# Kernel optimization log

Hardware: AMD Instinct MI355X
Metric: run time of the kernel (lower is better)

The kernel has to match this reference:

```python
import jax, jax.numpy as jnp
import numpy as np

N_HEADS, BUCKET, N_HASHES, DIM = 8, 25, 4, 128
PKM_TOPK = 16
NEG = -1e9
SELF_VAL = -5e4

def layer_norm(x, g, b, eps=1e-5):
    m = jnp.mean(x, -1, keepdims=True)
    v = jnp.mean(jnp.square(x - m), -1, keepdims=True)
    return (x - m) * jax.lax.rsqrt(v + eps) * g + b

def pos_encoding(S, d):
    pos = jnp.arange(S, dtype=jnp.float32)[:, None]
    div = jnp.exp(jnp.arange(0, d, 2, dtype=jnp.float32) * (-9.21034037198 / d))
    pe = jnp.zeros((S, d), jnp.float32)
    pe = pe.at[:, 0::2].set(jnp.sin(pos * div))
    pe = pe.at[:, 1::2].set(jnp.cos(pos * div))
    return pe

def look_back(t):
    # concat each chunk with the previous chunk along the within-chunk axis
    return jnp.concatenate([t, jnp.roll(t, 1, axis=1)], axis=2)

def lsh_attend(qk, v, keep, rot):
    # qk, v: [BH, S, D]; keep: [BH, S] bool; rot: [D, R, n_buckets//2]
    BH, S, D = qk.shape
    R = rot.shape[1]
    nb = 2 * rot.shape[2]
    kn = qk * jax.lax.rsqrt(jnp.sum(jnp.square(qk), -1, keepdims=True) + 1e-9)  # shared-QK keys are unit length
    rotated = jnp.einsum('bsd,drn->brsn', qk, rot)
    buckets = jnp.argmax(jnp.concatenate([rotated, -rotated], -1), axis=-1)  # [BH, R, S]
    buckets = buckets + (jnp.arange(R) * nb)[None, :, None]  # offset per hash round
    buckets = buckets.reshape(BH, R * S)
    pos = jnp.arange(R * S) % S
    perm = jnp.argsort(buckets * S + pos[None, :], axis=-1)  # stable sort by (bucket, position)
    undo = jnp.argsort(perm, axis=-1)
    st = perm % S  # original token position of each sorted slot
    gather = lambda t: jnp.take_along_axis(t, st[:, :, None], axis=1)
    c = BUCKET
    nc = (R * S) // c
    sq = gather(qk).reshape(BH, nc, c, D)
    sk = gather(kn).reshape(BH, nc, c, D)
    sv = gather(v).reshape(BH, nc, c, D)
    sm = jnp.take_along_axis(keep, st, axis=1).reshape(BH, nc, c)
    t_q = st.reshape(BH, nc, c)
    bk, bv = look_back(sk), look_back(sv)
    t_kv, m_kv = look_back(t_q), look_back(sm)
    dots = jnp.einsum('bncd,bnkd->bnck', sq, bk) * (D ** -0.5)  # [BH, nc, c, 2c]
    pair = sm[..., :, None] & m_kv[..., None, :]
    dots = jnp.where(pair, dots, NEG)                                   # padding mask
    dots = jnp.where(t_q[..., :, None] < t_kv[..., None, :], NEG, dots)  # causal
    dots = jnp.where(t_q[..., :, None] == t_kv[..., None, :], SELF_VAL, dots)  # discourage self-attn
    lse = jax.nn.logsumexp(dots, axis=-1, keepdims=True)
    attn = jnp.exp(dots - lse)
    bo = jnp.einsum('bnck,bnkd->bncd', attn, bv)
    so = bo.reshape(BH, R * S, D)
    slse = lse.reshape(BH, R * S)
    o = jnp.take_along_axis(so, undo[:, :, None], axis=1).reshape(BH, R, S, D)
    lu = jnp.take_along_axis(slse, undo, axis=1).reshape(BH, R, S)
    w = jax.nn.softmax(lu, axis=1)[..., None]  # combine hash rounds by their logsumexp
    return jnp.sum(o * w, axis=1)

def lsh_self_attention(x, keep, Wqk, Wv, Wo, bo, rot):
    B, S, dim = x.shape
    H = N_HEADS
    Dh = dim // H
    split = lambda t: t.reshape(B, S, H, Dh).transpose(0, 2, 1, 3).reshape(B * H, S, Dh)
    qk, v = split(x @ Wqk), split(x @ Wv)
    keep_bh = jnp.repeat(keep, H, axis=0)
    o = lsh_attend(qk, v, keep_bh, rot)
    o = o.reshape(B, H, S, Dh).transpose(0, 2, 1, 3).reshape(B, S, dim)
    return o @ Wo + bo

def pkm(x, Wq, keys, values):
    # keys: [H, nk, 2, dh]; values: [nk*nk, dim] (product-key memory)
    B, S, dim = x.shape
    H, nk, _, dh = keys.shape
    q = (x @ Wq).reshape(B, S, H, 2, dh)
    dots = jnp.einsum('bshpd,hnpd->bshpn', q, keys)
    sx, ix = jax.lax.top_k(dots[..., 0, :], PKM_TOPK)
    sy, iy = jax.lax.top_k(dots[..., 1, :], PKM_TOPK)
    alls = (sx[..., :, None] + sy[..., None, :]).reshape(B, S, H, PKM_TOPK * PKM_TOPK)
    alli = (ix[..., :, None] * nk + iy[..., None, :]).reshape(B, S, H, PKM_TOPK * PKM_TOPK)
    fs, p = jax.lax.top_k(alls, PKM_TOPK)
    fi = jnp.take_along_axis(alli, p, axis=-1)
    attn = jax.nn.softmax(fs, -1)
    return jnp.einsum('bshk,bshkd->bsd', attn, values[fi])

def model_forward(fl, xi):
    (emb_mcc, emb_amt, emb_hour, emb_wday, rot, ln1_g, ln1_b, ln2_g, ln2_b,
     Wqk, Wv, Wo, bo, ff_w1, ff_b1, ff_w2, ff_b2, pkm_wq, pkm_keys, pkm_values,
     norm_g, norm_b, hw1, hb1, hw2_mcc, hb2_mcc, hw2_amt, hb2_amt,
     hw2_hour, hb2_hour, hw2_wday, hb2_wday) = fl
    x_mcc, x_amt, x_hour, x_wday = xi
    B, S = x_mcc.shape
    emb = jnp.concatenate([emb_mcc[x_mcc], emb_amt[x_amt], emb_hour[x_hour], emb_wday[x_wday]], axis=-1)
    emb = emb + pos_encoding(S, DIM)[None]
    keep = x_mcc != 0
    # reversible reformer: x1 = x1 + attn(ln(x2)); x2 = x2 + ff_or_pkm(ln(x1)); out = mean of halves
    x1 = x2 = emb
    ffi = pki = 0
    for l in range(8):
        h = layer_norm(x2, ln1_g[l], ln1_b[l])
        x1 = x1 + lsh_self_attention(h, keep, Wqk[l], Wv[l], Wo[l], bo[l], rot)
        h2 = layer_norm(x1, ln2_g[l], ln2_b[l])
        if l in (3, 6):  # pkm_layers = (4, 7), 1-indexed
            x2 = x2 + pkm(h2, pkm_wq[pki], pkm_keys[pki], pkm_values[pki])
            pki += 1
        else:
            x2 = x2 + (jax.nn.gelu(h2 @ ff_w1[ffi] + ff_b1[ffi], approximate=False) @ ff_w2[ffi] + ff_b2[ffi])
            ffi += 1
    y = layer_norm((x1 + x2) * 0.5, norm_g, norm_b)
    outs = []
    for i, (w2, b2) in enumerate([(hw2_mcc, hb2_mcc), (hw2_amt, hb2_amt), (hw2_hour, hb2_hour), (hw2_wday, hb2_wday)]):
        h = jax.nn.gelu(y @ hw1[i] + hb1[i], approximate=False)
        outs.append(h @ w2 + b2)
    return tuple(outs)

def setup_inputs() -> dict:
    key = jax.random.key(0)
    ks = iter(jax.random.split(key, 64))
    B, S = 16, 1000
    nrm = lambda *s: jax.random.normal(next(ks), s, jnp.float32) * 0.02
    inp = dict(
        x_mcc=jax.random.randint(next(ks), (B, S), 0, 350),
        x_amt=jax.random.randint(next(ks), (B, S), 0, 100),
        x_hour=jax.random.randint(next(ks), (B, S), 0, 25),
        x_wday=jax.random.randint(next(ks), (B, S), 0, 8),
        emb_mcc=nrm(350, 64), emb_amt=nrm(100, 32), emb_hour=nrm(25, 16), emb_wday=nrm(8, 16),
        rot=jax.random.normal(next(ks), (16, N_HASHES, 20), jnp.float32),  # [dim_head, rounds, n_buckets//2]
        ln1_g=jnp.ones((8, 128)), ln1_b=jnp.zeros((8, 128)),
        ln2_g=jnp.ones((8, 128)), ln2_b=jnp.zeros((8, 128)),
        Wqk=nrm(8, 128, 128), Wv=nrm(8, 128, 128), Wo=nrm(8, 128, 128), bo=jnp.zeros((8, 128)),
        ff_w1=nrm(6, 128, 512), ff_b1=jnp.zeros((6, 512)), ff_w2=nrm(6, 512, 128), ff_b2=jnp.zeros((6, 128)),
        pkm_wq=nrm(2, 128, 512), pkm_keys=nrm(2, 4, 128, 2, 64), pkm_values=nrm(2, 16384, 128),
        norm_g=jnp.ones((128,)), norm_b=jnp.zeros((128,)),
        hw1=nrm(4, 128, 128), hb1=jnp.zeros((4, 128)),
        hw2_mcc=nrm(128, 350), hb2_mcc=jnp.zeros((350,)),
        hw2_amt=nrm(128, 100), hb2_amt=jnp.zeros((100,)),
        hw2_hour=nrm(128, 25), hb2_hour=jnp.zeros((25,)),
        hw2_wday=nrm(128, 8), hb2_wday=jnp.zeros((8,)),
    )
    return inp

def reference(x_mcc, x_amt, x_hour, x_wday, emb_mcc, emb_amt, emb_hour, emb_wday, rot,
              ln1_g, ln1_b, ln2_g, ln2_b, Wqk, Wv, Wo, bo,
              ff_w1, ff_b1, ff_w2, ff_b2, pkm_wq, pkm_keys, pkm_values,
              norm_g, norm_b, hw1, hb1, hw2_mcc, hb2_mcc, hw2_amt, hb2_amt,
              hw2_hour, hb2_hour, hw2_wday, hb2_wday):
    fl = (emb_mcc, emb_amt, emb_hour, emb_wday, rot, ln1_g, ln1_b, ln2_g, ln2_b,
          Wqk, Wv, Wo, bo, ff_w1, ff_b1, ff_w2, ff_b2, pkm_wq, pkm_keys, pkm_values,
          norm_g, norm_b, hw1, hb1, hw2_mcc, hb2_mcc, hw2_amt, hb2_amt,
          hw2_hour, hb2_hour, hw2_wday, hb2_wday)
    return model_forward(fl, (x_mcc, x_amt, x_hour, x_wday))
```

## Files before the change

### kernel.cpp

```cpp
#include <hip/hip_runtime.h>
#include <math.h>

#define MM_GELU 1
#define MM_RES 2
#define MM_SPLIT 4

typedef __attribute__((ext_vector_type(8))) short bfrag;
typedef __attribute__((ext_vector_type(4))) float f32x4;

__device__ inline unsigned short f2bf_rne(float f) {
  unsigned u = __float_as_uint(f);
  unsigned r = u + 0x7FFFu + ((u >> 16) & 1u);
  return (unsigned short)(r >> 16);
}
__device__ inline float bf2f(unsigned short h) {
  return __uint_as_float(((unsigned)h) << 16);
}

__global__ __launch_bounds__(128) void embed_kernel(
    const int* __restrict__ xm, const int* __restrict__ xa,
    const int* __restrict__ xh, const int* __restrict__ xw,
    const float* __restrict__ em, const float* __restrict__ ea,
    const float* __restrict__ eh, const float* __restrict__ ew,
    float* __restrict__ x1, float* __restrict__ x2) {
  int row = blockIdx.x;
  int d = threadIdx.x;
  int s = row % 1000;
  float v;
  if (d < 64)       v = em[xm[row]*64 + d];
  else if (d < 96)  v = ea[xa[row]*32 + (d-64)];
  else if (d < 112) v = eh[xh[row]*16 + (d-96)];
  else              v = ew[xw[row]*16 + (d-112)];
  int i = d >> 1;
  float dv = expf((float)(2*i) * (-9.21034037198f/128.f));
  float ang = (float)s * dv;
  v += (d & 1) ? cosf(ang) : sinf(ang);
  x1[row*128 + d] = v;
  x2[row*128 + d] = v;
}

__global__ __launch_bounds__(256) void ln_kernel(
    const float* __restrict__ x, const float* __restrict__ xb,
    const float* __restrict__ g, const float* __restrict__ b,
    float* __restrict__ out) {
  int row = blockIdx.x * 4 + (threadIdx.x >> 6);
  int t = threadIdx.x & 63;
  float v0 = x[row*128 + t], v1 = x[row*128 + 64 + t];
  if (xb) { v0 = 0.5f*(v0 + xb[row*128 + t]); v1 = 0.5f*(v1 + xb[row*128 + 64 + t]); }
  float sum = v0 + v1;
  #pragma unroll
  for (int o = 32; o > 0; o >>= 1) sum += __shfl_xor(sum, o);
  float mean = sum * (1.f/128.f);
  float d0 = v0 - mean, d1 = v1 - mean;
  float vs = d0*d0 + d1*d1;
  #pragma unroll
  for (int o = 32; o > 0; o >>= 1) vs += __shfl_xor(vs, o);
  float rstd = rsqrtf(vs*(1.f/128.f) + 1e-5f);
  out[row*128 + t]      = d0*rstd*g[t]    + b[t];
  out[row*128 + 64 + t] = d1*rstd*g[t+64] + b[t+64];
}

__global__ __launch_bounds__(256) void mfma_matmul_kernel(
    const float* __restrict__ A, const float* __restrict__ W,
    const float* __restrict__ bias, float* __restrict__ C,
    int M, int N, int K, int flags) {
  __shared__ __align__(16) unsigned short Ah[64*40], Al[64*40], Bh[64*40], Bl[64*40];
  int tid = threadIdx.x;
  int bm = blockIdx.x * 64, bn = blockIdx.y * 64;
  int w = tid >> 6, lane = tid & 63;
  int l15 = lane & 15, kg = lane >> 4;
  f32x4 acc[4];
  #pragma unroll
  for (int t = 0; t < 4; ++t) { acc[t][0]=0.f; acc[t][1]=0.f; acc[t][2]=0.f; acc[t][3]=0.f; }
  int arr = tid >> 2, akc = (tid & 3) * 8;
  int bcol = tid >> 2, bk0 = (tid & 3) * 8;

  for (int k0 = 0; k0 < K; k0 += 32) {
    {
      const float* ap = A + (size_t)(bm + arr) * K + k0 + akc;
      float4 fa = *(const float4*)(ap);
      float4 fb = *(const float4*)(ap + 4);
      float av8[8] = {fa.x, fa.y, fa.z, fa.w, fb.x, fb.y, fb.z, fb.w};
      bfrag vh, vl;
      #pragma unroll
      for (int j = 0; j < 8; ++j) {
        unsigned short h = f2bf_rne(av8[j]);
        vh[j] = (short)h;
        vl[j] = (short)f2bf_rne(av8[j] - bf2f(h));
      }
      *(bfrag*)&Ah[arr*40 + akc] = vh;
      *(bfrag*)&Al[arr*40 + akc] = vl;
    }
    {
      int c = bn + bcol;
      float bv8[8];
      #pragma unroll
      for (int j = 0; j < 8; ++j) {
        int kk = k0 + bk0 + j;
        bv8[j] = (c < N) ? W[(size_t)kk * N + c] : 0.f;
      }
      #pragma unroll
      for (int j = 0; j < 8; j += 2) {
        unsigned short h0 = f2bf_rne(bv8[j]),   h1 = f2bf_rne(bv8[j+1]);
        unsigned short l0 = f2bf_rne(bv8[j]   - bf2f(h0));
        unsigned short l1 = f2bf_rne(bv8[j+1] - bf2f(h1));
        *(unsigned*)&Bh[bcol*40 + bk0 + j] = ((unsigned)h1 << 16) | h0;
        *(unsigned*)&Bl[bcol*40 + bk0 + j] = ((unsigned)l1 << 16) | l0;
      }
    }
    __syncthreads();
    int am = w*16 + l15;
    bfrag a_h = *(const bfrag*)&Ah[am*40 + kg*8];
    bfrag a_l = *(const bfrag*)&Al[am*40 + kg*8];
    #pragma unroll
    for (int t = 0; t < 4; ++t) {
      int nn = t*16 + l15;
      bfrag b_h = *(const bfrag*)&Bh[nn*40 + kg*8];
      bfrag b_l = *(const bfrag*)&Bl[nn*40 + kg*8];
      acc[t] = __builtin_amdgcn_mfma_f32_16x16x32_bf16(a_h, b_h, acc[t], 0, 0, 0);
      acc[t] = __builtin_amdgcn_mfma_f32_16x16x32_bf16(a_h, b_l, acc[t], 0, 0, 0);
      acc[t] = __builtin_amdgcn_mfma_f32_16x16x32_bf16(a_l, b_h, acc[t], 0, 0, 0);
    }
    __syncthreads();
  }
  #pragma unroll
  for (int t = 0; t < 4; ++t) {
    int col = bn + t*16 + l15;
    if (col < N) {
      #pragma unroll
      for (int r = 0; r < 4; ++r) {
        int row = bm + w*16 + kg*4 + r;
        float val = acc[t][r];
        if (bias) val += bias[col];
        if (flags & MM_GELU) val = 0.5f*val*(1.f + erff(val*0.70710678118f));
        size_t oi;
        if (flags & MM_SPLIT) {
          int bb = row / 1000, ss = row % 1000;
          int hd = col >> 4, dd = col & 15;
          oi = (((size_t)(bb*8 + hd))*1000 + ss)*16 + dd;
        } else {
          oi = (size_t)row*N + col;
        }
        if (flags & MM_RES) C[oi] += val; else C[oi] = val;
      }
    }
  }
}

__global__ __launch_bounds__(256) void bucket_kernel(
    const float* __restrict__ qk, const float* __restrict__ rot,
    int* __restrict__ buckets) {
  int idx = blockIdx.x*256 + threadIdx.x;
  if (idx >= 128000) return;
  int bh = idx / 1000, s = idx % 1000;
  float q[16];
  #pragma unroll
  for (int d = 0; d < 16; ++d) q[d] = qk[(bh*1000+s)*16 + d];
  #pragma unroll 1
  for (int r = 0; r < 4; ++r) {
    float rv[20];
    #pragma unroll
    for (int n = 0; n < 20; ++n) {
      float acc = 0.f;
      #pragma unroll
      for (int d = 0; d < 16; ++d) acc += q[d]*rot[(d*4 + r)*20 + n];
      rv[n] = acc;
    }
    float best = -INFINITY; int bi = 0;
    #pragma unroll
    for (int n = 0; n < 40; ++n) {
      float val = (n < 20) ? rv[n] : -rv[n-20];
      if (val > best) { best = val; bi = n; }
    }
    buckets[(bh*4 + r)*1000 + s] = bi;
  }
}

__global__ __launch_bounds__(64) void sort_kernel(
    const int* __restrict__ buckets, int* __restrict__ st, int* __restrict__ undo) {
  int bh = blockIdx.x >> 2;
  int r = blockIdx.x & 3;
  const int* bkt = buckets + (bh*4 + r)*1000;
  __shared__ int off[40];
  int lane = threadIdx.x;
  if (lane < 40) off[lane] = 0;
  __syncthreads();
  unsigned long long below = (lane == 63) ? 0x7FFFFFFFFFFFFFFFull : ((1ull << lane) - 1ull);
  for (int c = 0; c < 16; ++c) {
    int s = c*64 + lane;
    bool valid = (s < 1000);
    int b = valid ? bkt[s] : 0;
    unsigned long long mask = __ballot(valid);
    #pragma unroll
    for (int bit = 0; bit < 6; ++bit) {
      unsigned long long vote = __ballot((b >> bit) & 1);
      mask &= ((b >> bit) & 1) ? vote : ~vote;
    }
    if (valid) {
      int rank = (int)__popcll(mask & below);
      if (rank == 0) off[b] += (int)__popcll(mask);
    }
    __syncthreads();
  }
  if (lane == 0) {
    int acc = 0;
    for (int bb = 0; bb < 40; ++bb) { int cn = off[bb]; off[bb] = acc; acc += cn; }
  }
  __syncthreads();
  int base = bh*4000 + r*1000;
  for (int c = 0; c < 16; ++c) {
    int s = c*64 + lane;
    bool valid = (s < 1000);
    int b = valid ? bkt[s] : 0;
    unsigned long long mask = __ballot(valid);
    #pragma unroll
    for (int bit = 0; bit < 6; ++bit) {
      unsigned long long vote = __ballot((b >> bit) & 1);
      mask &= ((b >> bit) & 1) ? vote : ~vote;
    }
    if (valid) {
      int myoff = off[b];
      int rank = (int)__popcll(mask & below);
      int slot = myoff + rank;
      st[base + slot] = s;
      undo[base + s] = r*1000 + slot;
      if (rank == 0) off[b] = myoff + (int)__popcll(mask);
    }
    __syncthreads();
  }
}

__global__ __launch_bounds__(64) void attn_chunk_kernel(
    const float* __restrict__ qk, const float* __restrict__ v,
    const int* __restrict__ st, const int* __restrict__ xm,
    float* __restrict__ so, float* __restrict__ slse) {
  int blk = blockIdx.x;
  int bh = blk / 160;
  int n = blk % 160;
  int b = bh >> 3;
  int lane = threadIdx.x;
  __shared__ __align__(16) float RAW[50][20];
  __shared__ __align__(16) float BV[50][20];
  __shared__ float RSQ[50];
  __shared__ int TKV[50], MKV[50];
  int pn = (n + 159) % 160;
  if (lane < 50) {
    int slot = (lane < 25) ? (n*25 + lane) : (pn*25 + (lane - 25));
    int t = st[bh*4000 + slot];
    TKV[lane] = t;
    MKV[lane] = (xm[b*1000 + t] != 0) ? 1 : 0;
  }
  __syncthreads();
  for (int e = lane; e < 200; e += 64) {
    int rr = e >> 2, j = (e & 3) * 4;
    int t = TKV[rr];
    const float* qr = qk + ((size_t)bh*1000 + t)*16 + j;
    const float* vr = v  + ((size_t)bh*1000 + t)*16 + j;
    *(float4*)&RAW[rr][j] = *(const float4*)qr;
    *(float4*)&BV[rr][j]  = *(const float4*)vr;
  }
  __syncthreads();
  if (lane < 50) {
    float ss = 1e-9f;
    #pragma unroll
    for (int d = 0; d < 16; ++d) ss += RAW[lane][d]*RAW[lane][d];
    RSQ[lane] = rsqrtf(ss);
  }
  __syncthreads();
  if (lane < 50) {
    int q = lane % 25, h = lane / 25;
    int partner = (h == 0) ? lane + 25 : lane - 25;
    float sq[16];
    #pragma unroll
    for (int j = 0; j < 4; ++j) {
      float4 f = *(const float4*)&RAW[q][j*4];
      sq[j*4+0]=f.x; sq[j*4+1]=f.y; sq[j*4+2]=f.z; sq[j*4+3]=f.w;
    }
    int tq = TKV[q], mq = MKV[q];
    float p[25];
    #pragma unroll
    for (int i = 0; i < 25; ++i) {
      int k = h*25 + i;
      float acc = 0.f;
      #pragma unroll
      for (int j = 0; j < 4; ++j) {
        float4 f = *(const float4*)&RAW[k][j*4];
        acc += sq[j*4+0]*f.x + sq[j*4+1]*f.y + sq[j*4+2]*f.z + sq[j*4+3]*f.w;
      }
      acc *= 0.25f * RSQ[k];
      int tk = TKV[k], mk = MKV[k];
      if (!(mq && mk)) acc = -1e9f;
      if (tq < tk) acc = -1e9f;
      if (tq == tk) acc = -5e4f;
      p[i] = acc;
    }
    float m = -INFINITY;
    #pragma unroll
    for (int i = 0; i < 25; ++i) m = fmaxf(m, p[i]);
    m = fmaxf(m, __shfl(m, partner));
    float S = 0.f;
    #pragma unroll
    for (int i = 0; i < 25; ++i) { p[i] = expf(p[i] - m); S += p[i]; }
    S += __shfl(S, partner);
    float lse = m + logf(S);
    float rS = 1.f / S;
    float o[16];
    #pragma unroll
    for (int d = 0; d < 16; ++d) o[d] = 0.f;
    #pragma unroll
    for (int i = 0; i < 25; ++i) {
      int k = h*25 + i;
      float wt = p[i];
      #pragma unroll
      for (int j = 0; j < 4; ++j) {
        float4 f = *(const float4*)&BV[k][j*4];
        o[j*4+0] += wt*f.x; o[j*4+1] += wt*f.y; o[j*4+2] += wt*f.z; o[j*4+3] += wt*f.w;
      }
    }
    #pragma unroll
    for (int d = 0; d < 16; ++d) o[d] += __shfl(o[d], partner);
    if (h == 0) {
      int slot = n*25 + q;
      float* op = so + ((size_t)bh*4000 + slot)*16;
      #pragma unroll
      for (int j = 0; j < 4; ++j) {
        float4 f;
        f.x = o[j*4+0]*rS; f.y = o[j*4+1]*rS; f.z = o[j*4+2]*rS; f.w = o[j*4+3]*rS;
        *(float4*)(op + j*4) = f;
      }
      slse[bh*4000 + slot] = lse;
    }
  }
}

__global__ __launch_bounds__(256) void combine_kernel(
    const float* __restrict__ so, const float* __restrict__ slse,
    const int* __restrict__ undo, float* __restrict__ ao) {
  int idx = blockIdx.x*256 + threadIdx.x;
  if (idx >= 2048000) return;
  int d = idx & 15;
  int s = (idx >> 4) % 1000;
  int bh = idx / 16000;
  int b = bh >> 3, hd = bh & 7;
  int s0 = undo[bh*4000 + s];
  int s1 = undo[bh*4000 + 1000 + s];
  int s2 = undo[bh*4000 + 2000 + s];
  int s3 = undo[bh*4000 + 3000 + s];
  float l0 = slse[bh*4000 + s0], l1 = slse[bh*4000 + s1];
  float l2 = slse[bh*4000 + s2], l3 = slse[bh*4000 + s3];
  float m = fmaxf(fmaxf(l0,l1), fmaxf(l2,l3));
  float w0 = expf(l0-m), w1 = expf(l1-m), w2 = expf(l2-m), w3 = expf(l3-m);
  float rs = 1.f/(w0+w1+w2+w3);
  const float* base = so + (size_t)bh*4000*16;
  float o = w0*base[s0*16+d] + w1*base[s1*16+d] + w2*base[s2*16+d] + w3*base[s3*16+d];
  ao[((size_t)b*1000 + s)*128 + hd*16 + d] = o * rs;
}

__global__ __launch_bounds__(256) void pkm_m_kernel(
    const float* __restrict__ Wq, const float* __restrict__ keys,
    float* __restrict__ M) {
  int hp = blockIdx.x;
  int h = hp >> 1, p = hp & 1;
  int tid = threadIdx.x;
  __shared__ float Ks[128][65];
  for (int e = tid; e < 8192; e += 256) {
    int n = e >> 6, d = e & 63;
    Ks[n][d] = keys[((size_t)(h*128 + n)*2 + p)*64 + d];
  }
  __syncthreads();
  int k = tid >> 1;
  int nbase = (tid & 1) * 64;
  float wk[64];
  const float* wq = Wq + (size_t)k*512 + h*128 + p*64;
  #pragma unroll
  for (int d = 0; d < 64; ++d) wk[d] = wq[d];
  for (int n = 0; n < 64; ++n) {
    int nn = nbase + n;
    float acc = 0.f;
    #pragma unroll
    for (int d = 0; d < 64; ++d) acc += wk[d]*Ks[nn][d];
    M[(size_t)k*1024 + hp*128 + nn] = acc;
  }
}

__device__ inline unsigned long long pk_key(float v, int idx) {
  unsigned u = __float_as_uint(v);
  u = (u & 0x80000000u) ? ~u : (u | 0x80000000u);
  unsigned kv = ~u;
  return ((unsigned long long)kv << 32) | (unsigned)idx;
}
__device__ inline float pk_val(unsigned long long key) {
  unsigned m = ~(unsigned)(key >> 32);
  return (m & 0x80000000u) ? __uint_as_float(m & 0x7FFFFFFFu) : __uint_as_float(~m);
}

__global__ __launch_bounds__(512) void pkm_select_kernel(
    const float* __restrict__ dots, const float* __restrict__ values,
    float* __restrict__ x2out) {
  int row = blockIdx.x;
  int tid = threadIdx.x;
  int w = tid >> 6;
  int lane = tid & 63;
  int h = w >> 1, p = w & 1;
  __shared__ float SVAL[4][2][16];
  __shared__ int SIDX[4][2][16];
  __shared__ float OUT[4][128];
  const float* dr = dots + (size_t)row*1024 + h*256 + p*128;
  {
    unsigned long long k0 = pk_key(dr[lane], lane);
    unsigned long long k1 = pk_key(dr[64 + lane], 64 + lane);
    #pragma unroll 1
    for (int k = 2; k <= 128; k <<= 1) {
      #pragma unroll 1
      for (int j = k >> 1; j >= 1; j >>= 1) {
        if (j == 64) {
          unsigned long long lo = (k0 < k1) ? k0 : k1;
          unsigned long long hi = (k0 < k1) ? k1 : k0;
          k0 = lo; k1 = hi;
        } else {
          unsigned long long p0 = __shfl_xor(k0, j);
          unsigned long long p1 = __shfl_xor(k1, j);
          bool low = ((lane & j) == 0);
          bool up0 = ((lane & k) == 0);
          bool up1 = (((lane + 64) & k) == 0);
          bool t0 = (low == up0) ? (p0 < k0) : (p0 > k0);
          bool t1 = (low == up1) ? (p1 < k1) : (p1 > k1);
          if (t0) k0 = p0;
          if (t1) k1 = p1;
        }
      }
    }
    if (lane < 16) {
      SVAL[h][p][lane] = pk_val(k0);
      SIDX[h][p][lane] = (int)(unsigned)(k0 & 0xFFFFFFFFull);
    }
  }
  __syncthreads();
  if (p == 0) {
    int kx, ky;
    if      (lane < 16) { kx = 0; ky = lane; }
    else if (lane < 24) { kx = 1; ky = lane - 16; }
    else if (lane < 29) { kx = 2; ky = lane - 24; }
    else if (lane < 33) { kx = 3; ky = lane - 29; }
    else if (lane < 36) { kx = 4; ky = lane - 33; }
    else if (lane < 38) { kx = 5; ky = lane - 36; }
    else if (lane < 40) { kx = 6; ky = lane - 38; }
    else if (lane < 42) { kx = 7; ky = lane - 40; }
    else                { kx = 8 + (lane - 42); ky = 0; }
    unsigned long long key;
    if (lane < 50) {
      float cv = SVAL[h][0][kx] + SVAL[h][1][ky];
      key = pk_key(cv, kx*16 + ky);
    } else {
      key = ~0ull;
    }
    #pragma unroll 1
    for (int k = 2; k <= 64; k <<= 1) {
      #pragma unroll 1
      for (int j = k >> 1; j >= 1; j >>= 1) {
        unsigned long long pk = __shfl_xor(key, j);
        bool low = ((lane & j) == 0);
        bool up = ((lane & k) == 0);
        bool take = (low == up) ? (pk < key) : (pk > key);
        if (take) key = pk;
      }
    }
    float myv = pk_val(key);
    int pos = (int)(key & 0xFFull);
    int myfi = SIDX[h][0][pos >> 4] * 128 + SIDX[h][1][pos & 15];
    float fs0 = __shfl(myv, 0);
    float osum0 = 0.f, osum1 = 0.f, wsum = 0.f;
    #pragma unroll
    for (int k = 0; k < 16; ++k) {
      float fv = __shfl(myv, k);
      int fik = __shfl(myfi, k);
      float wgk = expf(fv - fs0);
      wsum += wgk;
      const float* vr = values + (size_t)fik * 128;
      osum0 += wgk * vr[lane];
      osum1 += wgk * vr[lane + 64];
    }
    float rs = 1.f / wsum;
    OUT[h][lane] = osum0 * rs;
    OUT[h][lane + 64] = osum1 * rs;
  }
  __syncthreads();
  if (tid < 128) {
    float r = OUT[0][tid] + OUT[1][tid] + OUT[2][tid] + OUT[3][tid];
    x2out[(size_t)row*128 + tid] += r;
  }
}

extern "C" void kernel_launch(void* const* d_in, const int* in_sizes, int n_in,
                              void* d_out, int out_size, void* d_ws, size_t ws_size,
                              hipStream_t stream) {
  (void)in_sizes; (void)n_in; (void)out_size; (void)ws_size;
  const int* x_mcc  = (const int*)d_in[0];
  const int* x_amt  = (const int*)d_in[1];
  const int* x_hour = (const int*)d_in[2];
  const int* x_wday = (const int*)d_in[3];
  const float* emb_mcc  = (const float*)d_in[4];
  const float* emb_amt  = (const float*)d_in[5];
  const float* emb_hour = (const float*)d_in[6];
  const float* emb_wday = (const float*)d_in[7];
  const float* rot   = (const float*)d_in[8];
  const float* ln1_g = (const float*)d_in[9];
  const float* ln1_b = (const float*)d_in[10];
  const float* ln2_g = (const float*)d_in[11];
  const float* ln2_b = (const float*)d_in[12];
  const float* Wqk = (const float*)d_in[13];
  const float* Wv  = (const float*)d_in[14];
  const float* Wo  = (const float*)d_in[15];
  const float* bo  = (const float*)d_in[16];
  const float* ff_w1 = (const float*)d_in[17];
  const float* ff_b1 = (const float*)d_in[18];
  const float* ff_w2 = (const float*)d_in[19];
  const float* ff_b2 = (const float*)d_in[20];
  const float* pkm_wq   = (const float*)d_in[21];
  const float* pkm_keys = (const float*)d_in[22];
  const float* pkm_vals = (const float*)d_in[23];
  const float* norm_g = (const float*)d_in[24];
  const float* norm_b = (const float*)d_in[25];
  const float* hw1 = (const float*)d_in[26];
  const float* hb1 = (const float*)d_in[27];

  float* ws = (float*)d_ws;
  float* x1v  = ws;
  float* x2v  = ws + 2048000;
  float* hbuf = ws + 4096000;
  float* scrA = ws + 6144000;
  float* qk     = scrA;
  float* vv     = scrA + 2048000;
  float* so     = scrA + 4096000;
  float* slse   = scrA + 12288000;
  int*   buckets= (int*)(scrA + 12800000);
  int*   stp    = (int*)(scrA + 13312000);
  int*   undo   = (int*)(scrA + 13824000);
  float* attn_o = scrA + 14336000;
  float* big    = scrA;
  float* dotsb  = scrA;
  float* Mbuf   = ws + 22528000;

  embed_kernel<<<16000, 128, 0, stream>>>(x_mcc, x_amt, x_hour, x_wday,
      emb_mcc, emb_amt, emb_hour, emb_wday, x1v, x2v);

  int ffi = 0, pki = 0;
  for (int l = 0; l < 8; ++l) {
    ln_kernel<<<4000, 256, 0, stream>>>(x2v, nullptr, ln1_g + l*128, ln1_b + l*128, hbuf);
    { dim3 g(250, 2); mfma_matmul_kernel<<<g, 256, 0, stream>>>(hbuf, Wqk + (size_t)l*16384, nullptr, qk, 16000, 128, 128, MM_SPLIT); }
    { dim3 g(250, 2); mfma_matmul_kernel<<<g, 256, 0, stream>>>(hbuf, Wv  + (size_t)l*16384, nullptr, vv, 16000, 128, 128, MM_SPLIT); }
    bucket_kernel<<<500, 256, 0, stream>>>(qk, rot, buckets);
    sort_kernel<<<512, 64, 0, stream>>>(buckets, stp, undo);
    attn_chunk_kernel<<<20480, 64, 0, stream>>>(qk, vv, stp, x_mcc, so, slse);
    combine_kernel<<<8000, 256, 0, stream>>>(so, slse, undo, attn_o);
    { dim3 g(250, 2); mfma_matmul_kernel<<<g, 256, 0, stream>>>(attn_o, Wo + (size_t)l*16384, bo + l*128, x1v, 16000, 128, 128, MM_RES); }
    ln_kernel<<<4000, 256, 0, stream>>>(x1v, nullptr, ln2_g + l*128, ln2_b + l*128, hbuf);
    if (l == 3 || l == 6) {
      pkm_m_kernel<<<8, 256, 0, stream>>>(pkm_wq + (size_t)pki*65536, pkm_keys + (size_t)pki*65536, Mbuf);
      { dim3 g(250, 16); mfma_matmul_kernel<<<g, 256, 0, stream>>>(hbuf, Mbuf, nullptr, dotsb, 16000, 1024, 128, 0); }
      pkm_select_kernel<<<16000, 512, 0, stream>>>(dotsb, pkm_vals + (size_t)pki*2097152, x2v);
      ++pki;
    } else {
      { dim3 g(250, 8); mfma_matmul_kernel<<<g, 256, 0, stream>>>(hbuf, ff_w1 + (size_t)ffi*65536, ff_b1 + ffi*512, big, 16000, 512, 128, MM_GELU); }
      { dim3 g(250, 2); mfma_matmul_kernel<<<g, 256, 0, stream>>>(big, ff_w2 + (size_t)ffi*65536, ff_b2 + ffi*128, x2v, 16000, 128, 512, MM_RES); }
      ++ffi;
    }
  }
  ln_kernel<<<4000, 256, 0, stream>>>(x1v, x2v, norm_g, norm_b, hbuf);

  float* out = (float*)d_out;
  float* hid = scrA;
  const float* w2s[4] = {(const float*)d_in[28], (const float*)d_in[30], (const float*)d_in[32], (const float*)d_in[34]};
  const float* b2s[4] = {(const float*)d_in[29], (const float*)d_in[31], (const float*)d_in[33], (const float*)d_in[35]};
  const int ns[4] = {350, 100, 25, 8};
  size_t ooff = 0;
  for (int i = 0; i < 4; ++i) {
    { dim3 g(250, 2); mfma_matmul_kernel<<<g, 256, 0, stream>>>(hbuf, hw1 + (size_t)i*16384, hb1 + i*128, hid, 16000, 128, 128, MM_GELU); }
    { dim3 g(250, (unsigned)((ns[i]+63)/64)); mfma_matmul_kernel<<<g, 256, 0, stream>>>(hid, w2s[i], b2s[i], out + ooff, 16000, ns[i], 128, 0); }
    ooff += (size_t)16000 * ns[i];
  }
}
```

Before: 2.557 ms.

## Pre-split weights and activations into bf16 hi/lo, transpose weights, simplify PKM select

```diff
diff --git a/kernel.cpp b/kernel.cpp
--- a/kernel.cpp
+++ b/kernel.cpp
@@ -4,6 +4,7 @@
 #define MM_GELU 1
 #define MM_RES 2
 #define MM_SPLIT 4
+#define MM_SPLITONLY 8
 
 typedef __attribute__((ext_vector_type(8))) short bfrag;
 typedef __attribute__((ext_vector_type(4))) float f32x4;
@@ -42,7 +43,7 @@
 __global__ __launch_bounds__(256) void ln_kernel(
     const float* __restrict__ x, const float* __restrict__ xb,
     const float* __restrict__ g, const float* __restrict__ b,
-    float* __restrict__ out) {
+    unsigned short* __restrict__ oh, unsigned short* __restrict__ ol) {
   int row = blockIdx.x * 4 + (threadIdx.x >> 6);
   int t = threadIdx.x & 63;
   float v0 = x[row*128 + t], v1 = x[row*128 + 64 + t];
@@ -56,15 +57,52 @@
   #pragma unroll
   for (int o = 32; o > 0; o >>= 1) vs += __shfl_xor(vs, o);
   float rstd = rsqrtf(vs*(1.f/128.f) + 1e-5f);
-  out[row*128 + t]      = d0*rstd*g[t]    + b[t];
-  out[row*128 + 64 + t] = d1*rstd*g[t+64] + b[t+64];
-}
-
-__global__ __launch_bounds__(256) void mfma_matmul_kernel(
-    const float* __restrict__ A, const float* __restrict__ W,
+  float y0 = d0*rstd*g[t]    + b[t];
+  float y1 = d1*rstd*g[t+64] + b[t+64];
+  unsigned short h0 = f2bf_rne(y0), h1 = f2bf_rne(y1);
+  oh[row*128 + t]      = h0;
+  ol[row*128 + t]      = f2bf_rne(y0 - bf2f(h0));
+  oh[row*128 + 64 + t] = h1;
+  ol[row*128 + 64 + t] = f2bf_rne(y1 - bf2f(h1));
+}
+
+__global__ __launch_bounds__(256) void splitT_kernel(
+    const float* __restrict__ src, unsigned short* __restrict__ hiT,
+    unsigned short* __restrict__ loT, int K, int N,
+    long srcStride, long dstStride) {
+  src += (size_t)blockIdx.z * srcStride;
+  hiT += (size_t)blockIdx.z * dstStride;
+  loT += (size_t)blockIdx.z * dstStride;
+  int n0 = blockIdx.x * 64, k0 = blockIdx.y * 64;
+  __shared__ unsigned short sH[64][68], sL[64][68];
+  int tid = threadIdx.x;
+  int c = tid & 63, r4 = tid >> 6;
+  #pragma unroll
+  for (int rr = 0; rr < 16; ++rr) {
+    int r = r4 + rr*4;
+    float val = (n0 + c < N) ? src[(size_t)(k0 + r)*N + n0 + c] : 0.f;
+    unsigned short h = f2bf_rne(val);
+    sH[r][c] = h;
+    sL[r][c] = f2bf_rne(val - bf2f(h));
+  }
+  __syncthreads();
+  #pragma unroll
+  for (int rr = 0; rr < 16; ++rr) {
+    int n = r4 + rr*4;
+    if (n0 + n < N) {
+      hiT[(size_t)(n0 + n)*K + k0 + c] = sH[c][n];
+      loT[(size_t)(n0 + n)*K + k0 + c] = sL[c][n];
+    }
+  }
+}
+
+__global__ __launch_bounds__(256) void mm_bf16_kernel(
+    const unsigned short* __restrict__ Ah, const unsigned short* __restrict__ Al,
+    const unsigned short* __restrict__ BhT, const unsigned short* __restrict__ BlT,
     const float* __restrict__ bias, float* __restrict__ C,
+    unsigned short* __restrict__ Ch, unsigned short* __restrict__ Cl,
     int M, int N, int K, int flags) {
-  __shared__ __align__(16) unsigned short Ah[64*40], Al[64*40], Bh[64*40], Bl[64*40];
+  __shared__ __align__(16) unsigned short sAh[64][72], sAl[64][72], sBh[64][72], sBl[64][72];
   int tid = threadIdx.x;
   int bm = blockIdx.x * 64, bn = blockIdx.y * 64;
   int w = tid >> 6, lane = tid & 63;
@@ -72,54 +110,41 @@
   f32x4 acc[4];
   #pragma unroll
   for (int t = 0; t < 4; ++t) { acc[t][0]=0.f; acc[t][1]=0.f; acc[t][2]=0.f; acc[t][3]=0.f; }
-  int arr = tid >> 2, akc = (tid & 3) * 8;
-  int bcol = tid >> 2, bk0 = (tid & 3) * 8;
-
-  for (int k0 = 0; k0 < K; k0 += 32) {
-    {
-      const float* ap = A + (size_t)(bm + arr) * K + k0 + akc;
-      float4 fa = *(const float4*)(ap);
-      float4 fb = *(const float4*)(ap + 4);
-      float av8[8] = {fa.x, fa.y, fa.z, fa.w, fb.x, fb.y, fb.z, fb.w};
-      bfrag vh, vl;
+
+  for (int k0 = 0; k0 < K; k0 += 64) {
+    #pragma unroll
+    for (int uu = 0; uu < 2; ++uu) {
+      int u = tid + uu*256;
+      int rr = u >> 3, cc = u & 7;
+      size_t ga = (size_t)(bm + rr)*K + k0 + cc*8;
+      *(bfrag*)&sAh[rr][cc*8] = *(const bfrag*)(Ah + ga);
+      *(bfrag*)&sAl[rr][cc*8] = *(const bfrag*)(Al + ga);
+      int n = bn + rr;
+      if (n < N) {
+        size_t gb = (size_t)n*K + k0 + cc*8;
+        *(bfrag*)&sBh[rr][cc*8] = *(const bfrag*)(BhT + gb);
+        *(bfrag*)&sBl[rr][cc*8] = *(const bfrag*)(BlT + gb);
+      } else {
+        bfrag z = {0,0,0,0,0,0,0,0};
+        *(bfrag*)&sBh[rr][cc*8] = z;
+        *(bfrag*)&sBl[rr][cc*8] = z;
+      }
+    }
+    __syncthreads();
+    #pragma unroll
+    for (int ks = 0; ks < 2; ++ks) {
+      int am = w*16 + l15;
+      bfrag a_h = *(const bfrag*)&sAh[am][ks*32 + kg*8];
+      bfrag a_l = *(const bfrag*)&sAl[am][ks*32 + kg*8];
       #pragma unroll
-      for (int j = 0; j < 8; ++j) {
-        unsigned short h = f2bf_rne(av8[j]);
-        vh[j] = (short)h;
-        vl[j] = (short)f2bf_rne(av8[j] - bf2f(h));
+      for (int t = 0; t < 4; ++t) {
+        int nn = t*16 + l15;
+        bfrag b_h = *(const bfrag*)&sBh[nn][ks*32 + kg*8];
+        bfrag b_l = *(const bfrag*)&sBl[nn][ks*32 + kg*8];
+        acc[t] = __builtin_amdgcn_mfma_f32_16x16x32_bf16(a_h, b_h, acc[t], 0, 0, 0);
+        acc[t] = __builtin_amdgcn_mfma_f32_16x16x32_bf16(a_h, b_l, acc[t], 0, 0, 0);
+        acc[t] = __builtin_amdgcn_mfma_f32_16x16x32_bf16(a_l, b_h, acc[t], 0, 0, 0);
       }
-      *(bfrag*)&Ah[arr*40 + akc] = vh;
-      *(bfrag*)&Al[arr*40 + akc] = vl;
-    }
-    {
-      int c = bn + bcol;
-      float bv8[8];
-      #pragma unroll
-      for (int j = 0; j < 8; ++j) {
-        int kk = k0 + bk0 + j;
-        bv8[j] = (c < N) ? W[(size_t)kk * N + c] : 0.f;
-      }
-      #pragma unroll
-      for (int j = 0; j < 8; j += 2) {
-        unsigned short h0 = f2bf_rne(bv8[j]),   h1 = f2bf_rne(bv8[j+1]);
-        unsigned short l0 = f2bf_rne(bv8[j]   - bf2f(h0));
-        unsigned short l1 = f2bf_rne(bv8[j+1] - bf2f(h1));
-        *(unsigned*)&Bh[bcol*40 + bk0 + j] = ((unsigned)h1 << 16) | h0;
-        *(unsigned*)&Bl[bcol*40 + bk0 + j] = ((unsigned)l1 << 16) | l0;
-      }
-    }
-    __syncthreads();
-    int am = w*16 + l15;
-    bfrag a_h = *(const bfrag*)&Ah[am*40 + kg*8];
-    bfrag a_l = *(const bfrag*)&Al[am*40 + kg*8];
-    #pragma unroll
-    for (int t = 0; t < 4; ++t) {
-      int nn = t*16 + l15;
-      bfrag b_h = *(const bfrag*)&Bh[nn*40 + kg*8];
-      bfrag b_l = *(const bfrag*)&Bl[nn*40 + kg*8];
-      acc[t] = __builtin_amdgcn_mfma_f32_16x16x32_bf16(a_h, b_h, acc[t], 0, 0, 0);
-      acc[t] = __builtin_amdgcn_mfma_f32_16x16x32_bf16(a_h, b_l, acc[t], 0, 0, 0);
-      acc[t] = __builtin_amdgcn_mfma_f32_16x16x32_bf16(a_l, b_h, acc[t], 0, 0, 0);
     }
     __syncthreads();
   }
@@ -141,7 +166,12 @@
         } else {
           oi = (size_t)row*N + col;
         }
-        if (flags & MM_RES) C[oi] += val; else C[oi] = val;
+        if (flags & MM_SPLITONLY) {
+          unsigned short h = f2bf_rne(val);
+          Ch[oi] = h;
+          Cl[oi] = f2bf_rne(val - bf2f(h));
+        } else if (flags & MM_RES) C[oi] += val;
+        else C[oi] = val;
       }
     }
   }
@@ -335,7 +365,8 @@
 
 __global__ __launch_bounds__(256) void combine_kernel(
     const float* __restrict__ so, const float* __restrict__ slse,
-    const int* __restrict__ undo, float* __restrict__ ao) {
+    const int* __restrict__ undo, unsigned short* __restrict__ aoh,
+    unsigned short* __restrict__ aol) {
   int idx = blockIdx.x*256 + threadIdx.x;
   if (idx >= 2048000) return;
   int d = idx & 15;
@@ -352,8 +383,11 @@
   float w0 = expf(l0-m), w1 = expf(l1-m), w2 = expf(l2-m), w3 = expf(l3-m);
   float rs = 1.f/(w0+w1+w2+w3);
   const float* base = so + (size_t)bh*4000*16;
-  float o = w0*base[s0*16+d] + w1*base[s1*16+d] + w2*base[s2*16+d] + w3*base[s3*16+d];
-  ao[((size_t)b*1000 + s)*128 + hd*16 + d] = o * rs;
+  float o = (w0*base[s0*16+d] + w1*base[s1*16+d] + w2*base[s2*16+d] + w3*base[s3*16+d]) * rs;
+  size_t oi = ((size_t)b*1000 + s)*128 + hd*16 + d;
+  unsigned short h = f2bf_rne(o);
+  aoh[oi] = h;
+  aol[oi] = f2bf_rne(o - bf2f(h));
 }
 
 __global__ __launch_bounds__(256) void pkm_m_kernel(
@@ -394,96 +428,92 @@
   return (m & 0x80000000u) ? __uint_as_float(m & 0x7FFFFFFFu) : __uint_as_float(~m);
 }
 
-__global__ __launch_bounds__(512) void pkm_select_kernel(
+__global__ __launch_bounds__(256) void pkm_select_kernel(
     const float* __restrict__ dots, const float* __restrict__ values,
     float* __restrict__ x2out) {
   int row = blockIdx.x;
   int tid = threadIdx.x;
-  int w = tid >> 6;
+  int h = tid >> 6;
   int lane = tid & 63;
-  int h = w >> 1, p = w & 1;
-  __shared__ float SVAL[4][2][16];
-  __shared__ int SIDX[4][2][16];
   __shared__ float OUT[4][128];
-  const float* dr = dots + (size_t)row*1024 + h*256 + p*128;
-  {
-    unsigned long long k0 = pk_key(dr[lane], lane);
-    unsigned long long k1 = pk_key(dr[64 + lane], 64 + lane);
+  const float* dr = dots + (size_t)row*1024 + h*256;
+  unsigned long long x0 = pk_key(dr[lane], lane);
+  unsigned long long x1 = pk_key(dr[64 + lane], 64 + lane);
+  unsigned long long y0 = pk_key(dr[128 + lane], lane);
+  unsigned long long y1 = pk_key(dr[192 + lane], 64 + lane);
+  #pragma unroll 1
+  for (int k = 2; k <= 128; k <<= 1) {
     #pragma unroll 1
-    for (int k = 2; k <= 128; k <<= 1) {
-      #pragma unroll 1
-      for (int j = k >> 1; j >= 1; j >>= 1) {
-        if (j == 64) {
-          unsigned long long lo = (k0 < k1) ? k0 : k1;
-          unsigned long long hi = (k0 < k1) ? k1 : k0;
-          k0 = lo; k1 = hi;
-        } else {
-          unsigned long long p0 = __shfl_xor(k0, j);
-          unsigned long long p1 = __shfl_xor(k1, j);
-          bool low = ((lane & j) == 0);
-          bool up0 = ((lane & k) == 0);
-          bool up1 = (((lane + 64) & k) == 0);
-          bool t0 = (low == up0) ? (p0 < k0) : (p0 > k0);
-          bool t1 = (low == up1) ? (p1 < k1) : (p1 > k1);
-          if (t0) k0 = p0;
-          if (t1) k1 = p1;
-        }
+    for (int j = k >> 1; j >= 1; j >>= 1) {
+      if (j == 64) {
+        unsigned long long lo, hi;
+        lo = (x0 < x1) ? x0 : x1; hi = (x0 < x1) ? x1 : x0; x0 = lo; x1 = hi;
+        lo = (y0 < y1) ? y0 : y1; hi = (y0 < y1) ? y1 : y0; y0 = lo; y1 = hi;
+      } else {
+        unsigned long long px0 = __shfl_xor(x0, j);
+        unsigned long long px1 = __shfl_xor(x1, j);
+        unsigned long long py0 = __shfl_xor(y0, j);
+        unsigned long long py1 = __shfl_xor(y1, j);
+        bool low = ((lane & j) == 0);
+        bool up0 = ((lane & k) == 0);
+        bool up1 = (((lane + 64) & k) == 0);
+        bool d0 = (low == up0);
+        bool d1 = (low == up1);
+        if (d0 ? (px0 < x0) : (px0 > x0)) x0 = px0;
+        if (d1 ? (px1 < x1) : (px1 > x1)) x1 = px1;
+        if (d0 ? (py0 < y0) : (py0 > y0)) y0 = py0;
+        if (d1 ? (py1 < y1) : (py1 > y1)) y1 = py1;
       }
     }
-    if (lane < 16) {
-      SVAL[h][p][lane] = pk_val(k0);
-      SIDX[h][p][lane] = (int)(unsigned)(k0 & 0xFFFFFFFFull);
-    }
-  }
-  __syncthreads();
-  if (p == 0) {
-    int kx, ky;
-    if      (lane < 16) { kx = 0; ky = lane; }
-    else if (lane < 24) { kx = 1; ky = lane - 16; }
-    else if (lane < 29) { kx = 2; ky = lane - 24; }
-    else if (lane < 33) { kx = 3; ky = lane - 29; }
-    else if (lane < 36) { kx = 4; ky = lane - 33; }
-    else if (lane < 38) { kx = 5; ky = lane - 36; }
-    else if (lane < 40) { kx = 6; ky = lane - 38; }
-    else if (lane < 42) { kx = 7; ky = lane - 40; }
-    else                { kx = 8 + (lane - 42); ky = 0; }
-    unsigned long long key;
-    if (lane < 50) {
-      float cv = SVAL[h][0][kx] + SVAL[h][1][ky];
-      key = pk_key(cv, kx*16 + ky);
-    } else {
-      key = ~0ull;
-    }
+  }
+  float xv = pk_val(x0);
+  float yv = pk_val(y0);
+  int xi = (int)(unsigned)(x0 & 0xFFFFFFFFull);
+  int yi = (int)(unsigned)(y0 & 0xFFFFFFFFull);
+  int kx, ky;
+  if      (lane < 16) { kx = 0; ky = lane; }
+  else if (lane < 24) { kx = 1; ky = lane - 16; }
+  else if (lane < 29) { kx = 2; ky = lane - 24; }
+  else if (lane < 33) { kx = 3; ky = lane - 29; }
+  else if (lane < 36) { kx = 4; ky = lane - 33; }
+  else if (lane < 38) { kx = 5; ky = lane - 36; }
+  else if (lane < 40) { kx = 6; ky = lane - 38; }
+  else if (lane < 42) { kx = 7; ky = lane - 40; }
+  else                { kx = 8 + (lane - 42); ky = 0; }
+  float sxk = __shfl(xv, kx);
+  float syk = __shfl(yv, ky);
+  unsigned long long key = (lane < 50) ? pk_key(sxk + syk, kx*16 + ky) : ~0ull;
+  #pragma unroll 1
+  for (int k = 2; k <= 64; k <<= 1) {
     #pragma unroll 1
-    for (int k = 2; k <= 64; k <<= 1) {
-      #pragma unroll 1
-      for (int j = k >> 1; j >= 1; j >>= 1) {
-        unsigned long long pk = __shfl_xor(key, j);
-        bool low = ((lane & j) == 0);
-        bool up = ((lane & k) == 0);
-        bool take = (low == up) ? (pk < key) : (pk > key);
-        if (take) key = pk;
-      }
-    }
-    float myv = pk_val(key);
-    int pos = (int)(key & 0xFFull);
-    int myfi = SIDX[h][0][pos >> 4] * 128 + SIDX[h][1][pos & 15];
-    float fs0 = __shfl(myv, 0);
-    float osum0 = 0.f, osum1 = 0.f, wsum = 0.f;
-    #pragma unroll
-    for (int k = 0; k < 16; ++k) {
-      float fv = __shfl(myv, k);
-      int fik = __shfl(myfi, k);
-      float wgk = expf(fv - fs0);
-      wsum += wgk;
-      const float* vr = values + (size_t)fik * 128;
-      osum0 += wgk * vr[lane];
-      osum1 += wgk * vr[lane + 64];
-    }
-    float rs = 1.f / wsum;
-    OUT[h][lane] = osum0 * rs;
-    OUT[h][lane + 64] = osum1 * rs;
-  }
+    for (int j = k >> 1; j >= 1; j >>= 1) {
+      unsigned long long pk = __shfl_xor(key, j);
+      bool low = ((lane & j) == 0);
+      bool up = ((lane & k) == 0);
+      bool take = (low == up) ? (pk < key) : (pk > key);
+      if (take) key = pk;
+    }
+  }
+  float myv = pk_val(key);
+  int pos = (int)(key & 0xFFull);
+  int ix = __shfl(xi, pos >> 4);
+  int iy = __shfl(yi, pos & 15);
+  int myfi = ix*128 + iy;
+  float fs0 = __shfl(myv, 0);
+  float osum0 = 0.f, osum1 = 0.f, wsum = 0.f;
+  #pragma unroll
+  for (int k = 0; k < 16; ++k) {
+    float fv = __shfl(myv, k);
+    int fik = __shfl(myfi, k);
+    float wgk = expf(fv - fs0);
+    wsum += wgk;
+    const float* vr = values + (size_t)fik * 128;
+    osum0 += wgk * vr[lane];
+    osum1 += wgk * vr[lane + 64];
+  }
+  float rs = 1.f / wsum;
+  OUT[h][lane] = osum0 * rs;
+  OUT[h][lane + 64] = osum1 * rs;
   __syncthreads();
   if (tid < 128) {
     float r = OUT[0][tid] + OUT[1][tid] + OUT[2][tid] + OUT[3][tid];
@@ -537,46 +567,84 @@
   int*   stp    = (int*)(scrA + 13312000);
   int*   undo   = (int*)(scrA + 13824000);
   float* attn_o = scrA + 14336000;
-  float* big    = scrA;
   float* dotsb  = scrA;
   float* Mbuf   = ws + 22528000;
 
+  unsigned short* hbuf_h = (unsigned short*)hbuf;
+  unsigned short* hbuf_l = hbuf_h + 2048000;
+  unsigned short* ao_h = (unsigned short*)attn_o;
+  unsigned short* ao_l = ao_h + 2048000;
+  unsigned short* big_h = (unsigned short*)scrA;
+  unsigned short* big_l = big_h + 8192000;
+  unsigned short* hid_h = ao_h;
+  unsigned short* hid_l = ao_l;
+
+  unsigned short* wsp = (unsigned short*)(ws + 22700000);
+  unsigned short* WqkT_h = wsp;
+  unsigned short* WqkT_l = wsp + 131072;
+  unsigned short* WvT_h  = wsp + 262144;
+  unsigned short* WvT_l  = wsp + 393216;
+  unsigned short* WoT_h  = wsp + 524288;
+  unsigned short* WoT_l  = wsp + 655360;
+  unsigned short* f1T_h  = wsp + 786432;
+  unsigned short* f1T_l  = wsp + 1179648;
+  unsigned short* f2T_h  = wsp + 1572864;
+  unsigned short* f2T_l  = wsp + 1966080;
+  unsigned short* MT_h   = wsp + 2359296;
+  unsigned short* MT_l   = wsp + 2490368;
+  unsigned short* hw1T_h = wsp + 2621440;
+  unsigned short* hw1T_l = wsp + 2686976;
+  unsigned short* h2T_h  = wsp + 2752512;
+  unsigned short* h2T_l  = wsp + 2814336;
+
+  { dim3 g(2,2,8); splitT_kernel<<<g,256,0,stream>>>(Wqk, WqkT_h, WqkT_l, 128,128, 16384,16384); }
+  { dim3 g(2,2,8); splitT_kernel<<<g,256,0,stream>>>(Wv,  WvT_h,  WvT_l,  128,128, 16384,16384); }
+  { dim3 g(2,2,8); splitT_kernel<<<g,256,0,stream>>>(Wo,  WoT_h,  WoT_l,  128,128, 16384,16384); }
+  { dim3 g(8,2,6); splitT_kernel<<<g,256,0,stream>>>(ff_w1, f1T_h, f1T_l, 128,512, 65536,65536); }
+  { dim3 g(2,8,6); splitT_kernel<<<g,256,0,stream>>>(ff_w2, f2T_h, f2T_l, 512,128, 65536,65536); }
+  { dim3 g(2,2,4); splitT_kernel<<<g,256,0,stream>>>(hw1, hw1T_h, hw1T_l, 128,128, 16384,16384); }
+  const float* w2s[4] = {(const float*)d_in[28], (const float*)d_in[30], (const float*)d_in[32], (const float*)d_in[34]};
+  const float* b2s[4] = {(const float*)d_in[29], (const float*)d_in[31], (const float*)d_in[33], (const float*)d_in[35]};
+  const int ns[4] = {350, 100, 25, 8};
+  const long h2off[4] = {0, 44800, 57600, 60800};
+  for (int i = 0; i < 4; ++i) {
+    dim3 g((ns[i]+63)/64, 2, 1);
+    splitT_kernel<<<g,256,0,stream>>>(w2s[i], h2T_h + h2off[i], h2T_l + h2off[i], 128, ns[i], 0, 0);
+  }
+
   embed_kernel<<<16000, 128, 0, stream>>>(x_mcc, x_amt, x_hour, x_wday,
       emb_mcc, emb_amt, emb_hour, emb_wday, x1v, x2v);
 
   int ffi = 0, pki = 0;
   for (int l = 0; l < 8; ++l) {
-    ln_kernel<<<4000, 256, 0, stream>>>(x2v, nullptr, ln1_g + l*128, ln1_b + l*128, hbuf);
-    { dim3 g(250, 2); mfma_matmul_kernel<<<g, 256, 0, stream>>>(hbuf, Wqk + (size_t)l*16384, nullptr, qk, 16000, 128, 128, MM_SPLIT); }
-    { dim3 g(250, 2); mfma_matmul_kernel<<<g, 256, 0, stream>>>(hbuf, Wv  + (size_t)l*16384, nullptr, vv, 16000, 128, 128, MM_SPLIT); }
+    ln_kernel<<<4000, 256, 0, stream>>>(x2v, nullptr, ln1_g + l*128, ln1_b + l*128, hbuf_h, hbuf_l);
+    { dim3 g(250, 2); mm_bf16_kernel<<<g, 256, 0, stream>>>(hbuf_h, hbuf_l, WqkT_h + l*16384, WqkT_l + l*16384, nullptr, qk, nullptr, nullptr, 16000, 128, 128, MM_SPLIT); }
+    { dim3 g(250, 2); mm_bf16_kernel<<<g, 256, 0, stream>>>(hbuf_h, hbuf_l, WvT_h + l*16384, WvT_l + l*16384, nullptr, vv, nullptr, nullptr, 16000, 128, 128, MM_SPLIT); }
     bucket_kernel<<<500, 256, 0, stream>>>(qk, rot, buckets);
     sort_kernel<<<512, 64, 0, stream>>>(buckets, stp, undo);
     attn_chunk_kernel<<<20480, 64, 0, stream>>>(qk, vv, stp, x_mcc, so, slse);
-    combine_kernel<<<8000, 256, 0, stream>>>(so, slse, undo, attn_o);
-    { dim3 g(250, 2); mfma_matmul_kernel<<<g, 256, 0, stream>>>(attn_o, Wo + (size_t)l*16384, bo + l*128, x1v, 16000, 128, 128, MM_RES); }
-    ln_kernel<<<4000, 256, 0, stream>>>(x1v, nullptr, ln2_g + l*128, ln2_b + l*128, hbuf);
+    combine_kernel<<<8000, 256, 0, stream>>>(so, slse, undo, ao_h, ao_l);
+    { dim3 g(250, 2); mm_bf16_kernel<<<g, 256, 0, stream>>>(ao_h, ao_l, WoT_h + l*16384, WoT_l + l*16384, bo + l*128, x1v, nullptr, nullptr, 16000, 128, 128, MM_RES); }
+    ln_kernel<<<4000, 256, 0, stream>>>(x1v, nullptr, ln2_g + l*128, ln2_b + l*128, hbuf_h, hbuf_l);
     if (l == 3 || l == 6) {
       pkm_m_kernel<<<8, 256, 0, stream>>>(pkm_wq + (size_t)pki*65536, pkm_keys + (size_t)pki*65536, Mbuf);
-      { dim3 g(250, 16); mfma_matmul_kernel<<<g, 256, 0, stream>>>(hbuf, Mbuf, nullptr, dotsb, 16000, 1024, 128, 0); }
-      pkm_select_kernel<<<16000, 512, 0, stream>>>(dotsb, pkm_vals + (size_t)pki*2097152, x2v);
+      { dim3 g(16, 2, 1); splitT_kernel<<<g,256,0,stream>>>(Mbuf, MT_h, MT_l, 128, 1024, 0, 0); }
+      { dim3 g(250, 16); mm_bf16_kernel<<<g, 256, 0, stream>>>(hbuf_h, hbuf_l, MT_h, MT_l, nullptr, dotsb, nullptr, nullptr, 16000, 1024, 128, 0); }
+      pkm_select_kernel<<<16000, 256, 0, stream>>>(dotsb, pkm_vals + (size_t)pki*2097152, x2v);
       ++pki;
     } else {
-      { dim3 g(250, 8); mfma_matmul_kernel<<<g, 256, 0, stream>>>(hbuf, ff_w1 + (size_t)ffi*65536, ff_b1 + ffi*512, big, 16000, 512, 128, MM_GELU); }
-      { dim3 g(250, 2); mfma_matmul_kernel<<<g, 256, 0, stream>>>(big, ff_w2 + (size_t)ffi*65536, ff_b2 + ffi*128, x2v, 16000, 128, 512, MM_RES); }
+      { dim3 g(250, 8); mm_bf16_kernel<<<g, 256, 0, stream>>>(hbuf_h, hbuf_l, f1T_h + ffi*65536, f1T_l + ffi*65536, ff_b1 + ffi*512, nullptr, big_h, big_l, 16000, 512, 128, MM_GELU|MM_SPLITONLY); }
+      { dim3 g(250, 2); mm_bf16_kernel<<<g, 256, 0, stream>>>(big_h, big_l, f2T_h + ffi*65536, f2T_l + ffi*65536, ff_b2 + ffi*128, x2v, nullptr, nullptr, 16000, 128, 512, MM_RES); }
       ++ffi;
     }
   }
-  ln_kernel<<<4000, 256, 0, stream>>>(x1v, x2v, norm_g, norm_b, hbuf);
+  ln_kernel<<<4000, 256, 0, stream>>>(x1v, x2v, norm_g, norm_b, hbuf_h, hbuf_l);
 
   float* out = (float*)d_out;
-  float* hid = scrA;
-  const float* w2s[4] = {(const float*)d_in[28], (const float*)d_in[30], (const float*)d_in[32], (const float*)d_in[34]};
-  const float* b2s[4] = {(const float*)d_in[29], (const float*)d_in[31], (const float*)d_in[33], (const float*)d_in[35]};
-  const int ns[4] = {350, 100, 25, 8};
   size_t ooff = 0;
   for (int i = 0; i < 4; ++i) {
-    { dim3 g(250, 2); mfma_matmul_kernel<<<g, 256, 0, stream>>>(hbuf, hw1 + (size_t)i*16384, hb1 + i*128, hid, 16000, 128, 128, MM_GELU); }
-    { dim3 g(250, (unsigned)((ns[i]+63)/64)); mfma_matmul_kernel<<<g, 256, 0, stream>>>(hid, w2s[i], b2s[i], out + ooff, 16000, ns[i], 128, 0); }
+    { dim3 g(250, 2); mm_bf16_kernel<<<g, 256, 0, stream>>>(hbuf_h, hbuf_l, hw1T_h + i*16384, hw1T_l + i*16384, hb1 + i*128, nullptr, hid_h, hid_l, 16000, 128, 128, MM_GELU|MM_SPLITONLY); }
+    { dim3 g(250, (unsigned)((ns[i]+63)/64)); mm_bf16_kernel<<<g, 256, 0, stream>>>(hid_h, hid_l, h2T_h + h2off[i], h2T_l + h2off[i], b2s[i], out + ooff, nullptr, nullptr, 16000, ns[i], 128, 0); }
     ooff += (size_t)16000 * ns[i];
   }
 }
```

New measurement: 2.553 ms. About the same (-0.2%).
